# Optimization experiments

Measured on AMD Instinct MI355X. Metric: run time of the kernel, lower is better.

Reference implementation:

```python
import jax, jax.numpy as jnp
import numpy as np

B, T, C = 8, 2048, 1024
H = 4 * C
N_LAYER, LAYER_ID = 12, 2
K_CLAMP = 60.0
LN_EPS = 1e-5


def _ln(x, g, b):
    m = jnp.mean(x, axis=-1, keepdims=True)
    v = jnp.var(x, axis=-1, keepdims=True)
    return (x - m) * jax.lax.rsqrt(v + LN_EPS) * g + b


def _mix(x, time_mix, combined_mix):
    # x: (B,T,C). Causal shift (zeros at t=0), anti-causal shift (zeros at t=T-1).
    c = x.shape[-1]
    xm1 = jnp.pad(x[:, :-1], ((0, 0), (1, 0), (0, 0)))
    xp1 = jnp.pad(x[:, 1:], ((0, 0), (0, 1), (0, 0)))
    xc = jnp.concatenate([xm1[..., :c // 2], xp1[..., c // 2:]], axis=-1)
    return x * time_mix + xm1 * (1.0 - time_mix) + xc * combined_mix


def _wkv(time_decay, time_first, k, v):
    # RWKV WKV exponential-decay linear recurrence (the custom CUDA kernel).
    # k, v: (B,T,C); k > 0 (already clamped+exp'd).
    # y_t = (a_t + exp(u)*k_t*v_t) / (b_t + exp(u)*k_t)
    # a_{t+1} = exp(-exp(w))*a_t + k_t*v_t ; b likewise with v=1.
    ed = jnp.exp(-jnp.exp(time_decay))  # per-step channel decay, (C,)
    eu = jnp.exp(time_first)            # current-token bonus, (C,)

    def step(carry, kv_t):
        a, b = carry
        kt, vt = kv_t
        y = (a + eu * kt * vt) / (b + eu * kt)
        return (ed * a + kt * vt, ed * b + kt), y

    kT = jnp.swapaxes(k, 0, 1)  # (T,B,C)
    vT = jnp.swapaxes(v, 0, 1)
    z = jnp.zeros_like(kT[0])
    _, y = jax.lax.scan(step, (z, z), (kT, vT))
    return jnp.swapaxes(y, 0, 1)  # (B,T,C)


def _time_mix_block(x, time_mix, combined_mix, time_decay, time_first, Wk, Wv, Wr, Wo):
    xm = _mix(x, time_mix, combined_mix)
    k = jnp.exp(jnp.minimum(xm @ Wk.T, K_CLAMP))
    v = xm @ Wv.T
    r = xm @ Wr.T
    wkv = _wkv(time_decay, time_first, k, v)
    return (jax.nn.sigmoid(r) * wkv) @ Wo.T


def _channel_mix_block(x, time_mix, combined_mix, Fk, Fv, Fr):
    xm = _mix(x, time_mix, combined_mix)
    k = jnp.square(jax.nn.relu(xm @ Fk.T))
    kv = k @ Fv.T
    return jax.nn.sigmoid(xm @ Fr.T) * kv


def setup_inputs():
    key = jax.random.key(0)
    ks = jax.random.split(key, 9)
    s = 0.02
    x = jax.random.normal(ks[0], (B, T, C), jnp.float32)
    # time_decay init per the module (f1/f2 interpolation over layers)
    h = np.arange(C, dtype=np.float64)
    frac = (LAYER_ID - 1) / (N_LAYER - 2)
    f1 = 3.0 + frac * (1.2 - 3.0)
    f2 = 0.65 + frac * (0.4 - 0.65)
    decay_speed = np.power(f2, h / (C - 1) * 7.0) * f1
    tm = jnp.concatenate([jnp.zeros(C // 2), jnp.ones(C // 2)]).reshape(1, 1, C).astype(jnp.float32)
    return dict(
        x=x,
        ln1_g=jnp.ones((C,), jnp.float32), ln1_b=jnp.zeros((C,), jnp.float32),
        ln2_g=jnp.ones((C,), jnp.float32), ln2_b=jnp.zeros((C,), jnp.float32),
        att_time_mix=tm,
        att_combined_mix=jnp.full((1, 1, C), 0.01, jnp.float32),
        time_decay=jnp.asarray(np.log(decay_speed), jnp.float32),
        time_first=jnp.full((C,), float(np.log(0.3)), jnp.float32),
        Wk=jax.random.normal(ks[1], (C, C), jnp.float32) * s,
        Wv=jax.random.normal(ks[2], (C, C), jnp.float32) * s,
        Wr=jax.random.normal(ks[3], (C, C), jnp.float32) * s,
        Wo=jax.random.normal(ks[4], (C, C), jnp.float32) * s,
        ffn_time_mix=tm,
        ffn_combined_mix=jnp.full((1, 1, C), 0.01, jnp.float32),
        Fk=jax.random.normal(ks[5], (H, C), jnp.float32) * s,
        Fv=jax.random.normal(ks[6], (C, H), jnp.float32) * s,
        Fr=jax.random.normal(ks[7], (C, C), jnp.float32) * s,
    )


def reference(x, ln1_g, ln1_b, ln2_g, ln2_b, att_time_mix, att_combined_mix,
              time_decay, time_first, Wk, Wv, Wr, Wo,
              ffn_time_mix, ffn_combined_mix, Fk, Fv, Fr):
    x = _ln(x, ln1_g, ln1_b)
    x = x + _time_mix_block(x, att_time_mix, att_combined_mix, time_decay, time_first, Wk, Wv, Wr, Wo)
    x = _ln(x, ln2_g, ln2_b)
    x = x + _channel_mix_block(x, ffn_time_mix, ffn_combined_mix, Fk, Fv, Fr)
    return x
```

## Files before the change

kernel.cpp:

```cpp
#include <hip/hip_runtime.h>
#include <hip/hip_bf16.h>

typedef float f32x4 __attribute__((ext_vector_type(4)));
typedef __bf16 bf16x8 __attribute__((ext_vector_type(8)));
typedef __bf16 bf16x4 __attribute__((ext_vector_type(4)));

#define DEVI static __device__ __forceinline__

DEVI void glds16(const void* g, void* l) {
  __builtin_amdgcn_global_load_lds((__attribute__((address_space(1))) void*)g,
                                   (__attribute__((address_space(3))) void*)l, 16, 0, 0);
}

DEVI f32x4 load4(const float* p) { return *(const f32x4*)p; }
DEVI f32x4 load4(const __bf16* p) {
  bf16x4 v = *(const bf16x4*)p;
  f32x4 o = { (float)v[0], (float)v[1], (float)v[2], (float)v[3] };
  return o;
}
DEVI void store4(float* p, f32x4 v) { *(f32x4*)p = v; }
DEVI void store4(__bf16* p, f32x4 v) {
  bf16x4 o = { (__bf16)v[0], (__bf16)v[1], (__bf16)v[2], (__bf16)v[3] };
  *(bf16x4*)p = o;
}

__global__ void cvt_bf16(const float* __restrict__ in, __bf16* __restrict__ out, int n4) {
  int i = blockIdx.x * 256 + threadIdx.x;
  if (i < n4) {
    f32x4 v = *(const f32x4*)(in + (size_t)i * 4);
    store4(out + (size_t)i * 4, v);
  }
}

template <typename TIN, typename TOUT>
__global__ __launch_bounds__(256) void ln_kernel(const TIN* __restrict__ x,
    const float* __restrict__ gw, const float* __restrict__ bw,
    TOUT* __restrict__ out) {
  const size_t row = blockIdx.x;
  f32x4 v = load4(x + row * 1024 + threadIdx.x * 4);
  float s = v[0] + v[1] + v[2] + v[3];
  float q = v[0]*v[0] + v[1]*v[1] + v[2]*v[2] + v[3]*v[3];
#pragma unroll
  for (int o = 32; o > 0; o >>= 1) { s += __shfl_down(s, o); q += __shfl_down(q, o); }
  __shared__ float ss[4], qq[4];
  const int w = threadIdx.x >> 6, l = threadIdx.x & 63;
  if (l == 0) { ss[w] = s; qq[w] = q; }
  __syncthreads();
  s = ss[0] + ss[1] + ss[2] + ss[3];
  q = qq[0] + qq[1] + qq[2] + qq[3];
  const float mean = s * (1.0f / 1024.0f);
  const float var = q * (1.0f / 1024.0f) - mean * mean;
  const float rstd = rsqrtf(var + 1e-5f);
  f32x4 g4 = *(const f32x4*)(gw + threadIdx.x * 4);
  f32x4 b4 = *(const f32x4*)(bw + threadIdx.x * 4);
  f32x4 o;
#pragma unroll
  for (int j = 0; j < 4; ++j) o[j] = (v[j] - mean) * rstd * g4[j] + b4[j];
  store4(out + row * 1024 + threadIdx.x * 4, o);
}

template <typename TIN>
__global__ __launch_bounds__(256) void mix_kernel(const TIN* __restrict__ x,
    const float* __restrict__ tm, const float* __restrict__ cm,
    __bf16* __restrict__ out) {
  const int idx = blockIdx.x * 256 + threadIdx.x;
  const int t = (idx >> 8) & 2047;
  const int c = (idx & 255) * 4;
  const size_t base = ((size_t)(idx >> 8) << 10) + c;
  f32x4 xv = load4(x + base);
  f32x4 xm1 = {0.f, 0.f, 0.f, 0.f}, xp1 = {0.f, 0.f, 0.f, 0.f};
  if (t > 0)    xm1 = load4(x + base - 1024);
  if (t < 2047) xp1 = load4(x + base + 1024);
  f32x4 tm4 = *(const f32x4*)(tm + c);
  f32x4 cm4 = *(const f32x4*)(cm + c);
  f32x4 xc = (c < 512) ? xm1 : xp1;
  f32x4 o;
#pragma unroll
  for (int j = 0; j < 4; ++j)
    o[j] = xv[j] * tm4[j] + xm1[j] * (1.0f - tm4[j]) + xc[j] * cm4[j];
  store4(out + base, o);
}

__global__ __launch_bounds__(256) void wkv_part(const __bf16* __restrict__ k,
    const __bf16* __restrict__ v, const float* __restrict__ td,
    float* __restrict__ scA, float* __restrict__ scB) {
  const int gid = blockIdx.x * 256 + threadIdx.x;
  const int c = gid & 1023;
  const int j = (gid >> 10) & 31;
  const int b = gid >> 15;
  const float ed = expf(-expf(td[c]));
  float A = 0.f, Bv = 0.f;
  size_t off = ((size_t)(b * 2048 + j * 64) << 10) + c;
#pragma unroll 4
  for (int i = 0; i < 64; ++i, off += 1024) {
    const float kt = (float)k[off];
    const float kv = kt * (float)v[off];
    A = ed * A + kv;
    Bv = ed * Bv + kt;
  }
  scA[gid] = A;
  scB[gid] = Bv;
}

__global__ __launch_bounds__(256) void wkv_scan(const float* __restrict__ td,
    float* __restrict__ scA, float* __restrict__ scB) {
  const int gid = blockIdx.x * 256 + threadIdx.x;
  const int c = gid & 1023;
  const int b = gid >> 10;
  const float edL = expf(-expf(td[c]) * 64.0f);
  float a = 0.f, bb = 0.f;
  size_t off = ((size_t)b << 15) + c;
  for (int j = 0; j < 32; ++j, off += 1024) {
    const float Aj = scA[off], Bj = scB[off];
    scA[off] = a;
    scB[off] = bb;
    a = edL * a + Aj;
    bb = edL * bb + Bj;
  }
}

__global__ __launch_bounds__(256) void wkv_apply(const __bf16* __restrict__ k,
    const __bf16* __restrict__ v, const __bf16* __restrict__ sr,
    const float* __restrict__ td, const float* __restrict__ tf,
    const float* __restrict__ scA, const float* __restrict__ scB,
    __bf16* __restrict__ srw) {
  const int gid = blockIdx.x * 256 + threadIdx.x;
  const int c = gid & 1023;
  const int j = (gid >> 10) & 31;
  const int b = gid >> 15;
  const float ed = expf(-expf(td[c]));
  const float eu = expf(tf[c]);
  float a = scA[gid], bb = scB[gid];
  size_t off = ((size_t)(b * 2048 + j * 64) << 10) + c;
#pragma unroll 4
  for (int i = 0; i < 64; ++i, off += 1024) {
    const float kt = (float)k[off];
    const float vt = (float)v[off];
    const float kv = kt * vt;
    const float y = (a + eu * kv) / (bb + eu * kt);
    srw[off] = (__bf16)((float)sr[off] * y);
    a = ed * a + kv;
    bb = ed * bb + kt;
  }
}

enum { EPI_NONE = 0, EPI_EXP, EPI_SIG, EPI_RELU2, EPI_RESID, EPI_FINAL, EPI_KVR };

#define SCHED0() __builtin_amdgcn_sched_barrier(0)
#define SBAR() { __builtin_amdgcn_s_barrier(); SCHED0(); }
#define VMW0() { asm volatile("s_waitcnt vmcnt(0)" ::: "memory"); SCHED0(); }
#define LGKM(n) { asm volatile("s_waitcnt lgkmcnt(" #n ")" ::: "memory"); SCHED0(); }

template <int EPI>
__global__ __launch_bounds__(512, 2) void gemmk(
    const __bf16* __restrict__ A, const __bf16* __restrict__ W,
    void* outp, const void* res, const void* sig, const int N, const int K) {
  __shared__ __bf16 sA[2][16384];
  __shared__ __bf16 sB[2][16384];
  const int tid = threadIdx.x;
  const int w = tid >> 6, l = tid & 63;
  const int wm = w >> 2, wn = w & 3;

  const int nwg = gridDim.x * gridDim.y;
  int wg = blockIdx.y * gridDim.x + blockIdx.x;
  wg = (wg & 7) * (nwg >> 3) + (wg >> 3);
  const int m0 = (wg / gridDim.x) << 8;
  const int n0 = (wg % gridDim.x) << 8;

  const int lr = l >> 3;
  const int lc = (l & 7) ^ lr;
  const size_t gA = (size_t)(m0 + w * 8 + lr) * K + lc * 8;
  const size_t gB = (size_t)(n0 + wn * 64 + wm * 8 + lr) * K + lc * 8;
  const int ldsA = w * 512;
  const int ldsB = (wn * 64 + wm * 8) * 64;

  const int NTK = K >> 6;

#define STAGE_A(buf, kt, i) glds16(A + gA + (size_t)(i) * 64 * K + (size_t)(kt) * 64, &sA[buf][ldsA + (i) * 4096])
#define STAGE_B(buf, kt, j) glds16(W + gB + (size_t)(j) * 16 * K + (size_t)(kt) * 64, &sB[buf][ldsB + (j) * 1024])

  const int rA = (wm * 128 + (l & 15)) * 64;
  const int rB = (wn * 64 + (l & 15)) * 64;
  const int csw = l & 7;
  const int k0 = l >> 4;
#define LDA(buf, mi, kk) (*(const bf16x8*)&sA[buf][rA + (mi) * 1024 + ((((kk) * 4 + k0) ^ csw) << 3)])
#define LDB(buf, ni, kk) (*(const bf16x8*)&sB[buf][rB + (ni) * 1024 + ((((kk) * 4 + k0) ^ csw) << 3)])

  f32x4 acc[8][4] = {};

  STAGE_A(0, 0, 0); STAGE_A(0, 0, 1); STAGE_A(0, 0, 2); STAGE_A(0, 0, 3);
  STAGE_B(0, 0, 0); STAGE_B(0, 0, 1); STAGE_B(0, 0, 2); STAGE_B(0, 0, 3);

  for (int kt = 0; kt < NTK; ++kt) {
    const int buf = kt & 1, nb = buf ^ 1;
    const bool st = (kt + 1 < NTK);
    VMW0();
    SBAR();
    if (st) {
      STAGE_A(nb, kt + 1, 0); STAGE_A(nb, kt + 1, 1); STAGE_A(nb, kt + 1, 2); STAGE_A(nb, kt + 1, 3);
      STAGE_B(nb, kt + 1, 0); STAGE_B(nb, kt + 1, 1); STAGE_B(nb, kt + 1, 2); STAGE_B(nb, kt + 1, 3);
    }
    SCHED0();
    bf16x8 a0[4], a1[4], a2[4], a3[4], b0[4], b1[4];
#pragma unroll
    for (int i = 0; i < 4; ++i) a0[i] = LDA(buf, i, 0);
#pragma unroll
    for (int i = 0; i < 4; ++i) b0[i] = LDB(buf, i, 0);
    SCHED0();
#pragma unroll
    for (int i = 0; i < 4; ++i) a1[i] = LDA(buf, i + 4, 0);
    SCHED0();
    LGKM(4);
    __builtin_amdgcn_s_setprio(1);
#pragma unroll
    for (int mi = 0; mi < 4; ++mi)
#pragma unroll
      for (int ni = 0; ni < 4; ++ni)
        acc[mi][ni] = __builtin_amdgcn_mfma_f32_16x16x32_bf16(a0[mi], b0[ni], acc[mi][ni], 0, 0, 0);
    __builtin_amdgcn_s_setprio(0); SCHED0();
#pragma unroll
    for (int i = 0; i < 4; ++i) a2[i] = LDA(buf, i, 1);
#pragma unroll
    for (int i = 0; i < 4; ++i) b1[i] = LDB(buf, i, 1);
    SCHED0();
    LGKM(8);
    __builtin_amdgcn_s_setprio(1);
#pragma unroll
    for (int mi = 0; mi < 4; ++mi)
#pragma unroll
      for (int ni = 0; ni < 4; ++ni)
        acc[mi + 4][ni] = __builtin_amdgcn_mfma_f32_16x16x32_bf16(a1[mi], b0[ni], acc[mi + 4][ni], 0, 0, 0);
    __builtin_amdgcn_s_setprio(0); SCHED0();
#pragma unroll
    for (int i = 0; i < 4; ++i) a3[i] = LDA(buf, i + 4, 1);
    SCHED0();
    LGKM(4);
    __builtin_amdgcn_s_setprio(1);
#pragma unroll
    for (int mi = 0; mi < 4; ++mi)
#pragma unroll
      for (int ni = 0; ni < 4; ++ni)
        acc[mi][ni] = __builtin_amdgcn_mfma_f32_16x16x32_bf16(a2[mi], b1[ni], acc[mi][ni], 0, 0, 0);
    __builtin_amdgcn_s_setprio(0); SCHED0();
    LGKM(0);
    __builtin_amdgcn_s_setprio(1);
#pragma unroll
    for (int mi = 0; mi < 4; ++mi)
#pragma unroll
      for (int ni = 0; ni < 4; ++ni)
        acc[mi + 4][ni] = __builtin_amdgcn_mfma_f32_16x16x32_bf16(a3[mi], b1[ni], acc[mi + 4][ni], 0, 0, 0);
    __builtin_amdgcn_s_setprio(0);
  }

  const int rl = (l >> 4) << 2, cl = l & 15;
#pragma unroll
  for (int mi = 0; mi < 8; ++mi) {
#pragma unroll
    for (int ni = 0; ni < 4; ++ni) {
#pragma unroll
      for (int e = 0; e < 4; ++e) {
        const int r = m0 + (wm << 7) + mi * 16 + rl + e;
        const int cidx = n0 + (wn << 6) + ni * 16 + cl;
        const size_t idx = (size_t)r * N + cidx;
        const float vacc = acc[mi][ni][e];
        if constexpr (EPI == EPI_NONE) {
          ((__bf16*)outp)[idx] = (__bf16)vacc;
        } else if constexpr (EPI == EPI_EXP) {
          ((__bf16*)outp)[idx] = (__bf16)expf(fminf(vacc, 60.0f));
        } else if constexpr (EPI == EPI_SIG) {
          ((__bf16*)outp)[idx] = (__bf16)(1.0f / (1.0f + expf(-vacc)));
        } else if constexpr (EPI == EPI_RELU2) {
          const float rv = fmaxf(vacc, 0.0f);
          ((__bf16*)outp)[idx] = (__bf16)(rv * rv);
        } else if constexpr (EPI == EPI_RESID) {
          ((__bf16*)outp)[idx] = (__bf16)(vacc + (float)((const __bf16*)res)[idx]);
        } else if constexpr (EPI == EPI_FINAL) {
          ((float*)outp)[idx] = ((const float*)res)[idx] + (float)((const __bf16*)sig)[idx] * vacc;
        } else {
          const int sel = cidx >> 10;
          const size_t oidx = (size_t)r * 1024 + (cidx & 1023);
          if (sel == 0)      ((__bf16*)outp)[oidx] = (__bf16)expf(fminf(vacc, 60.0f));
          else if (sel == 1) ((__bf16*)const_cast<void*>(res))[oidx] = (__bf16)vacc;
          else               ((__bf16*)const_cast<void*>(sig))[oidx] = (__bf16)(1.0f / (1.0f + expf(-vacc)));
        }
      }
    }
  }
}

extern "C" void kernel_launch(void* const* d_in, const int* in_sizes, int n_in,
                              void* d_out, int out_size, void* d_ws, size_t ws_size,
                              hipStream_t stream) {
  (void)in_sizes; (void)n_in; (void)out_size;
  const float* x    = (const float*)d_in[0];
  const float* ln1g = (const float*)d_in[1];
  const float* ln1b = (const float*)d_in[2];
  const float* ln2g = (const float*)d_in[3];
  const float* ln2b = (const float*)d_in[4];
  const float* atm  = (const float*)d_in[5];
  const float* acm  = (const float*)d_in[6];
  const float* td   = (const float*)d_in[7];
  const float* tf   = (const float*)d_in[8];
  const float* Wk   = (const float*)d_in[9];
  const float* Wv   = (const float*)d_in[10];
  const float* Wr   = (const float*)d_in[11];
  const float* Wo   = (const float*)d_in[12];
  const float* ftm  = (const float*)d_in[13];
  const float* fcm  = (const float*)d_in[14];
  const float* Fk   = (const float*)d_in[15];
  const float* Fv   = (const float*)d_in[16];
  const float* Fr   = (const float*)d_in[17];

  constexpr size_t C = 1024, T = 2048, Bs = 8, H = 4096;
  constexpr size_t NT = Bs * T;
  constexpr size_t NTC = NT * C;
  constexpr size_t CC = C * C;
  constexpr size_t CH = C * H;

  char* p = (char*)d_ws;
  auto takeb = [&](size_t elems) { __bf16* q = (__bf16*)p; p += elems * 2; return q; };
  __bf16* wKVR = takeb(3 * CC);
  __bf16* wWo  = takeb(CC);
  __bf16* wFk  = takeb(CH);
  __bf16* wFv  = takeb(CH);
  __bf16* wFr  = takeb(CC);
  __bf16* Ab   = takeb(NTC);
  __bf16* Bb   = takeb(NTC);
  __bf16* Db   = takeb(NTC);
  float* scA = (float*)p; p += Bs * 32 * C * 4;
  float* scB = (float*)p; p += Bs * 32 * C * 4;
  __bf16* kk = (__bf16*)p;
  const size_t used = (size_t)(p - (char*)d_ws);
  const size_t kkcap = ws_size > used ? ws_size - used : 0;
  int chunks = 4;
  if (kkcap >= NT * H * 2)          chunks = 1;
  else if (kkcap >= NT * H)         chunks = 2;
  __bf16* Cb = kk;
  __bf16* sr  = (__bf16*)d_out;
  float*  x3  = (float*)d_out;

  auto cvt = [&](const float* src, size_t n, __bf16* dst) {
    const int n4 = (int)(n / 4);
    cvt_bf16<<<dim3((n4 + 255) / 256), dim3(256), 0, stream>>>(src, dst, n4);
  };
  cvt(Wk, CC, wKVR); cvt(Wv, CC, wKVR + CC); cvt(Wr, CC, wKVR + 2 * CC);
  cvt(Wo, CC, wWo); cvt(Fk, CH, wFk); cvt(Fv, CH, wFv); cvt(Fr, CC, wFr);

  const dim3 blk(256), blkG(512);

  ln_kernel<float, __bf16><<<dim3((unsigned)NT), blk, 0, stream>>>(x, ln1g, ln1b, Ab);
  mix_kernel<__bf16><<<dim3((unsigned)(NTC / 1024)), blk, 0, stream>>>(Ab, atm, acm, Bb);
  gemmk<EPI_KVR><<<dim3(12, 64), blkG, 0, stream>>>(Bb, wKVR, Cb, Db, sr, 3072, 1024);
  wkv_part<<<dim3(1024), blk, 0, stream>>>(Cb, Db, td, scA, scB);
  wkv_scan<<<dim3(32), blk, 0, stream>>>(td, scA, scB);
  wkv_apply<<<dim3(1024), blk, 0, stream>>>(Cb, Db, sr, td, tf, scA, scB, Bb);
  gemmk<EPI_RESID><<<dim3(4, 64), blkG, 0, stream>>>(Bb, wWo, Ab, Ab, nullptr, 1024, 1024);
  ln_kernel<__bf16, float><<<dim3((unsigned)NT), blk, 0, stream>>>(Ab, ln2g, ln2b, x3);
  mix_kernel<float><<<dim3((unsigned)(NTC / 1024)), blk, 0, stream>>>(x3, ftm, fcm, Db);
  gemmk<EPI_SIG><<<dim3(4, 64), blkG, 0, stream>>>(Db, wFr, Bb, nullptr, nullptr, 1024, 1024);
  const size_t Mc = NT / chunks;
  for (int ch = 0; ch < chunks; ++ch) {
    const size_t ro = (size_t)ch * Mc;
    gemmk<EPI_RELU2><<<dim3(16, (unsigned)(Mc / 256)), blkG, 0, stream>>>(
        Db + ro * C, wFk, kk, nullptr, nullptr, 4096, 1024);
    gemmk<EPI_FINAL><<<dim3(4, (unsigned)(Mc / 256)), blkG, 0, stream>>>(
        kk, wFv, (float*)d_out + ro * C, (const float*)d_out + ro * C,
        Bb + ro * C, 1024, 4096);
  }
}
```

Before: 777.5 us.

## Interleave next-tile global-to-LDS loads across MFMA phases in GEMM loop

Restructures the GEMM main loop so the next K-tile's global-to-LDS loads are issued in four pairs spread between the four MFMA phases. Each phase now ends with a barrier and a partial vmcnt wait, replacing the single full drain at the top of each iteration. The aim is to overlap memory traffic with tensor-core work and avoid the vmcnt(0) stall. The cost is more workgroup barriers per iteration and lgkmcnt(0) waits before every MFMA group.

```diff
diff --git a/kernel.cpp b/kernel.cpp
--- a/kernel.cpp
+++ b/kernel.cpp
@@ -148,8 +148,8 @@
 
 #define SCHED0() __builtin_amdgcn_sched_barrier(0)
 #define SBAR() { __builtin_amdgcn_s_barrier(); SCHED0(); }
-#define VMW0() { asm volatile("s_waitcnt vmcnt(0)" ::: "memory"); SCHED0(); }
-#define LGKM(n) { asm volatile("s_waitcnt lgkmcnt(" #n ")" ::: "memory"); SCHED0(); }
+#define VMW(n) { asm volatile("s_waitcnt vmcnt(" #n ")" ::: "memory"); SCHED0(); }
+#define LGKM0() { asm volatile("s_waitcnt lgkmcnt(0)" ::: "memory"); SCHED0(); }
 
 template <int EPI>
 __global__ __launch_bounds__(512, 2) void gemmk(
@@ -188,29 +188,25 @@
 
   f32x4 acc[8][4] = {};
 
-  STAGE_A(0, 0, 0); STAGE_A(0, 0, 1); STAGE_A(0, 0, 2); STAGE_A(0, 0, 3);
   STAGE_B(0, 0, 0); STAGE_B(0, 0, 1); STAGE_B(0, 0, 2); STAGE_B(0, 0, 3);
+  STAGE_A(0, 0, 0); STAGE_A(0, 0, 2); STAGE_A(0, 0, 1); STAGE_A(0, 0, 3);
+  VMW(2);
+  SBAR();
 
   for (int kt = 0; kt < NTK; ++kt) {
     const int buf = kt & 1, nb = buf ^ 1;
     const bool st = (kt + 1 < NTK);
-    VMW0();
+    bf16x8 a0[4], a1[4], a2[4], a3[4], b0[4], b1[4];
+#pragma unroll
+    for (int i = 0; i < 4; ++i) b0[i] = LDB(buf, i, 0);
+#pragma unroll
+    for (int i = 0; i < 4; ++i) a0[i] = LDA(buf, i, 0);
+    SCHED0();
+    if (st) { STAGE_B(nb, kt + 1, 0); STAGE_B(nb, kt + 1, 1); }
+    SCHED0();
+    if (st) { VMW(2); } else { VMW(0); }
     SBAR();
-    if (st) {
-      STAGE_A(nb, kt + 1, 0); STAGE_A(nb, kt + 1, 1); STAGE_A(nb, kt + 1, 2); STAGE_A(nb, kt + 1, 3);
-      STAGE_B(nb, kt + 1, 0); STAGE_B(nb, kt + 1, 1); STAGE_B(nb, kt + 1, 2); STAGE_B(nb, kt + 1, 3);
-    }
-    SCHED0();
-    bf16x8 a0[4], a1[4], a2[4], a3[4], b0[4], b1[4];
-#pragma unroll
-    for (int i = 0; i < 4; ++i) a0[i] = LDA(buf, i, 0);
-#pragma unroll
-    for (int i = 0; i < 4; ++i) b0[i] = LDB(buf, i, 0);
-    SCHED0();
-#pragma unroll
-    for (int i = 0; i < 4; ++i) a1[i] = LDA(buf, i + 4, 0);
-    SCHED0();
-    LGKM(4);
+    LGKM0();
     __builtin_amdgcn_s_setprio(1);
 #pragma unroll
     for (int mi = 0; mi < 4; ++mi)
@@ -219,11 +215,14 @@
         acc[mi][ni] = __builtin_amdgcn_mfma_f32_16x16x32_bf16(a0[mi], b0[ni], acc[mi][ni], 0, 0, 0);
     __builtin_amdgcn_s_setprio(0); SCHED0();
 #pragma unroll
-    for (int i = 0; i < 4; ++i) a2[i] = LDA(buf, i, 1);
+    for (int i = 0; i < 4; ++i) a1[i] = LDA(buf, i + 4, 0);
 #pragma unroll
     for (int i = 0; i < 4; ++i) b1[i] = LDB(buf, i, 1);
     SCHED0();
-    LGKM(8);
+    if (st) { STAGE_B(nb, kt + 1, 2); STAGE_B(nb, kt + 1, 3); }
+    SCHED0();
+    SBAR();
+    LGKM0();
     __builtin_amdgcn_s_setprio(1);
 #pragma unroll
     for (int mi = 0; mi < 4; ++mi)
@@ -232,9 +231,12 @@
         acc[mi + 4][ni] = __builtin_amdgcn_mfma_f32_16x16x32_bf16(a1[mi], b0[ni], acc[mi + 4][ni], 0, 0, 0);
     __builtin_amdgcn_s_setprio(0); SCHED0();
 #pragma unroll
-    for (int i = 0; i < 4; ++i) a3[i] = LDA(buf, i + 4, 1);
-    SCHED0();
-    LGKM(4);
+    for (int i = 0; i < 4; ++i) a2[i] = LDA(buf, i, 1);
+    SCHED0();
+    if (st) { STAGE_A(nb, kt + 1, 0); STAGE_A(nb, kt + 1, 2); }
+    SCHED0();
+    SBAR();
+    LGKM0();
     __builtin_amdgcn_s_setprio(1);
 #pragma unroll
     for (int mi = 0; mi < 4; ++mi)
@@ -242,14 +244,21 @@
       for (int ni = 0; ni < 4; ++ni)
         acc[mi][ni] = __builtin_amdgcn_mfma_f32_16x16x32_bf16(a2[mi], b1[ni], acc[mi][ni], 0, 0, 0);
     __builtin_amdgcn_s_setprio(0); SCHED0();
-    LGKM(0);
+#pragma unroll
+    for (int i = 0; i < 4; ++i) a3[i] = LDA(buf, i + 4, 1);
+    SCHED0();
+    if (st) { STAGE_A(nb, kt + 1, 1); STAGE_A(nb, kt + 1, 3); }
+    SCHED0();
+    if (st) { VMW(2); }
+    SBAR();
+    LGKM0();
     __builtin_amdgcn_s_setprio(1);
 #pragma unroll
     for (int mi = 0; mi < 4; ++mi)
 #pragma unroll
       for (int ni = 0; ni < 4; ++ni)
         acc[mi + 4][ni] = __builtin_amdgcn_mfma_f32_16x16x32_bf16(a3[mi], b1[ni], acc[mi + 4][ni], 0, 0, 0);
-    __builtin_amdgcn_s_setprio(0);
+    __builtin_amdgcn_s_setprio(0); SCHED0();
   }
 
   const int rl = (l >> 4) << 2, cl = l & 15;
```

After: 724.6 us. -6.8%, faster.
